# Performance work log

Hardware: AMD Instinct MI355X
Metric: run time of the kernel (lower is better)

Reference implementation:

```python
import jax, jax.numpy as jnp
import numpy as np

# Dims: N batch, C=in=out channels, T frames, V joints, S subsets, R rel_channels, H SE hidden
N, C, T, V = 256, 64, 64, 25
S, R = 3, C // 8           # num_subset, rel_channels = in_channels // rel_reduction
O = C                       # out_channels
H = max(4, O // 4)          # SE attention_channels
BN_EPS = 1e-5


def setup_inputs() -> dict:
    key = jax.random.key(0)
    ks = jax.random.split(key, 12)
    sc = 0.1
    return {
        "x":     jax.random.normal(ks[0], (N, C, T, V), jnp.float32),
        "PA":    jax.random.normal(ks[1], (S, V, V), jnp.float32) * sc,
        "alpha": jnp.ones((S,), jnp.float32),
        # per-subset stacked 1x1-conv weights (kernel_size=1 -> plain matrices)
        "w1": jax.random.normal(ks[2], (S, R, C), jnp.float32) * (2.0 / C) ** 0.5,
        "b1": jnp.zeros((S, R), jnp.float32),
        "w2": jax.random.normal(ks[3], (S, R, C), jnp.float32) * (2.0 / C) ** 0.5,
        "b2": jnp.zeros((S, R), jnp.float32),
        "w3": jax.random.normal(ks[4], (S, O, C), jnp.float32) * (2.0 / C) ** 0.5,
        "b3": jnp.zeros((S, O), jnp.float32),
        "w4": jax.random.normal(ks[5], (S, O, R), jnp.float32) * (2.0 / R) ** 0.5,
        "b4": jnp.zeros((S, O), jnp.float32),
        # final BN (eval mode: running_mean=0, running_var=1)
        "bn_w": jnp.ones((O,), jnp.float32),
        "bn_b": jnp.zeros((O,), jnp.float32),
        # SE channel attention
        "se_w1": jax.random.normal(ks[6], (H, O), jnp.float32) * (2.0 / O) ** 0.5,
        "se_b1": jnp.zeros((H,), jnp.float32),
        "se_w2": jax.random.normal(ks[7], (O, H), jnp.float32) * (2.0 / H) ** 0.5,
        "se_b2": jnp.zeros((O,), jnp.float32),
    }


def reference(x, PA, alpha, w1, b1, w2, b2, w3, b3, w4, b4,
              bn_w, bn_b, se_w1, se_b1, se_w2, se_b2):
    # --- CTRGC for all S subsets at once ---
    # conv1(x).mean(-2) == conv1 applied to x.mean over T (1x1 conv is linear)
    xm = x.mean(axis=2)                                            # [N,C,V]
    x1 = jnp.einsum('ncv,src->nsrv', xm, w1) + b1[None, :, :, None]
    x2 = jnp.einsum('ncv,src->nsrv', xm, w2) + b2[None, :, :, None]
    x3 = jnp.einsum('nctv,soc->nsotv', x, w3) + b3[None, :, :, None, None]
    # outer-difference + tanh attention map: [N,S,R,V(u),V(v)]
    att = jnp.tanh(x1[..., :, None] - x2[..., None, :])
    m = jnp.einsum('nsruv,sor->nsouv', att, w4) + b4[None, :, :, None, None]
    Asym = PA + jnp.swapaxes(PA, -1, -2)                           # A + A^T, [S,V,V]
    m = m * alpha[None, :, None, None, None] + Asym[None, :, None, :, :]
    m = jax.nn.softmax(m, axis=-2)                                 # softmax over u (dim=-2)
    # einsum 'ncuv,nctv->nctu' per subset, summed over subsets
    y = jnp.einsum('nsouv,nsotv->notu', m, x3)                     # [N,O,T,V]
    # --- BatchNorm2d (eval: mean 0, var 1) ---
    y = y / jnp.sqrt(1.0 + BN_EPS) * bn_w[None, :, None, None] + bn_b[None, :, None, None]
    # --- SE channel attention ---
    pooled = y.mean(axis=(2, 3))                                   # [N,O]
    h = jax.nn.relu(pooled @ se_w1.T + se_b1)
    se = jax.nn.sigmoid(h @ se_w2.T + se_b2)
    y = y * se[:, :, None, None]
    # --- residual (in==out -> identity down) + ReLU ---
    return jax.nn.relu(y + x)
```

## Files before the change

### kernel.cpp

```cpp
#include <hip/hip_runtime.h>

#define NN 256
#define CC 64
#define TT 64
#define VV 25
#define SS 3
#define RR 8
#define OO 64
#define HH 16

typedef _Float16 f16;
typedef _Float16 f16x8 __attribute__((ext_vector_type(8)));
typedef float f32x4 __attribute__((ext_vector_type(4)));

#define IBN 0.9999950000374997f

#define MG_NSTRIDE 153600

__device__ __forceinline__ float tanh_fast(float xx) {
  float e = __expf(2.0f * xx);
  return 1.0f - __fdividef(2.0f, e + 1.0f);
}

__device__ __forceinline__ int mti(int mo, int u, int v) {
  return (mo*800 + u*32 + v) ^ ((mo & 6) << 2);
}

__global__ __launch_bounds__(512) void k1(
    const float* __restrict__ x, const float* __restrict__ PA,
    const float* __restrict__ alpha,
    const float* __restrict__ w1, const float* __restrict__ b1,
    const float* __restrict__ w2, const float* __restrict__ b2,
    const float* __restrict__ w3, const float* __restrict__ b3,
    const float* __restrict__ w4, const float* __restrict__ b4,
    const float* __restrict__ bn_w, const float* __restrict__ bn_b,
    const float* __restrict__ se_w1, const float* __restrict__ se_b1,
    const float* __restrict__ se_w2, const float* __restrict__ se_b2,
    f16* __restrict__ m_g, float* __restrict__ se_g, f16* __restrict__ w3p_g)
{
  __shared__ float part[64][8][25];
  __shared__ float xms[1600];
  __shared__ float x1s[600], x2s[600];
  __shared__ float w1s[1536], w2s[1536];
  __shared__ float asym_s[1875];
  __shared__ __attribute__((aligned(16))) float att2[5000];
  __shared__ __attribute__((aligned(16))) f16 mtf[25600];
  __shared__ float xmv[64], pooledv[64], hbuf[16];

  int n = blockIdx.x, tid = threadIdx.x;

  for (int i = tid; i < 1536; i += 512) { w1s[i] = w1[i]; w2s[i] = w2[i]; }
  for (int i = tid; i < 1875; i += 512) {
    int s = i / 625, rem = i - s*625, u = rem / 25, v = rem - u*25;
    asym_s[i] = PA[s*625 + u*25 + v] + PA[s*625 + v*25 + u];
  }
  for (int i = tid; i < 5600; i += 512) {
    int mo = i / 175, rem = i - mo*175, u = rem / 7, v = 25 + (rem - u*7);
    mtf[mti(mo, u, v)] = (f16)0.f;
  }

  {
    int c = tid >> 3, tq = tid & 7;
    const float* p = x + (size_t)(n*64 + c)*1600 + tq*200;
    float acc[25];
    #pragma unroll
    for (int i = 0; i < 25; ++i) acc[i] = 0.f;
    for (int blk = 0; blk < 2; ++blk) {
      const float* pb = p + blk*100;
      #pragma unroll
      for (int j = 0; j < 25; ++j) {
        f32x4 vv = *(const f32x4*)(pb + 4*j);
        acc[(4*j + 0) % 25] += vv[0];
        acc[(4*j + 1) % 25] += vv[1];
        acc[(4*j + 2) % 25] += vv[2];
        acc[(4*j + 3) % 25] += vv[3];
      }
    }
    #pragma unroll
    for (int i = 0; i < 25; ++i) part[c][tq][i] = acc[i];
  }
  __syncthreads();

  for (int idx = tid; idx < 1600; idx += 512) {
    int cc = idx / 25, v = idx - cc*25;
    float s = 0.f;
    #pragma unroll
    for (int tq = 0; tq < 8; ++tq) s += part[cc][tq][v];
    xms[idx] = s * (1.0f/64.0f);
  }
  __syncthreads();

  for (int idx = tid; idx < 600; idx += 512) {
    int sr = idx / 25, v = idx - sr*25;
    float a1 = b1[sr], a2 = b2[sr];
    #pragma unroll
    for (int c = 0; c < 64; ++c) {
      float xv = xms[c*25 + v];
      a1 += xv * w1s[sr*64 + c];
      a2 += xv * w2s[sr*64 + c];
    }
    x1s[idx] = a1; x2s[idx] = a2;
  }

  if (tid < 64) {
    float s = 0.f;
    #pragma unroll
    for (int v = 0; v < 25; ++v) s += xms[tid*25 + v];
    xmv[tid] = s * (1.0f/25.0f);
  }
  __syncthreads();
  if (tid < 64) {
    int o = tid;
    float pp = b3[o] + b3[64 + o] + b3[128 + o];
    for (int cc = 0; cc < 64; ++cc)
      pp += xmv[cc] * (w3[o*64 + cc] + w3[4096 + o*64 + cc] + w3[8192 + o*64 + cc]);
    pooledv[o] = IBN * bn_w[o] * pp + bn_b[o];
  }
  __syncthreads();
  if (tid < 16) {
    float hh = se_b1[tid];
    for (int o = 0; o < 64; ++o) hh += pooledv[o] * se_w1[tid*64 + o];
    hbuf[tid] = fmaxf(hh, 0.0f);
  }
  __syncthreads();
  if (tid < 64) {
    float t = se_b2[tid];
    for (int j = 0; j < 16; ++j) t += hbuf[j] * se_w2[tid*16 + j];
    se_g[n*64 + tid] = 1.0f / (1.0f + __expf(-t));
  }

  f16x8* mg8 = (f16x8*)(m_g + (size_t)n*MG_NSTRIDE);
  for (int s = 0; s < 3; ++s) {
    __syncthreads();
    for (int idx = tid; idx < 5000; idx += 512) {
      int uv = idx >> 3, r = idx & 7;
      int u = uv / 25, v = uv - u*25;
      att2[idx] = tanh_fast(x1s[(s*8 + r)*25 + u] - x2s[(s*8 + r)*25 + v]);
    }
    __syncthreads();

    float alphav = alpha[s];
    for (int oh = 0; oh < 2; ++oh) {
      if (tid < 400) {
        int ot = tid / 25, v = tid - ot*25;
        int o0 = oh*32 + ot*2;
        float w4r[2][8], b4r[2];
        #pragma unroll
        for (int oo = 0; oo < 2; ++oo) {
          b4r[oo] = b4[s*64 + o0 + oo];
          #pragma unroll
          for (int r = 0; r < 8; ++r) w4r[oo][r] = w4[(s*64 + o0 + oo)*8 + r];
        }
        float acc[2][25];
        #pragma unroll
        for (int u = 0; u < 25; ++u) {
          const float* ap = &att2[(u*25 + v)*8];
          f32x4 a0 = *(const f32x4*)ap;
          f32x4 a1 = *(const f32x4*)(ap + 4);
          float asv = asym_s[s*625 + u*25 + v];
          #pragma unroll
          for (int oo = 0; oo < 2; ++oo) {
            float t = b4r[oo];
            t += a0[0]*w4r[oo][0] + a0[1]*w4r[oo][1] + a0[2]*w4r[oo][2] + a0[3]*w4r[oo][3];
            t += a1[0]*w4r[oo][4] + a1[1]*w4r[oo][5] + a1[2]*w4r[oo][6] + a1[3]*w4r[oo][7];
            acc[oo][u] = t*alphav + asv;
          }
        }
        #pragma unroll
        for (int oo = 0; oo < 2; ++oo) {
          int mo = ot*2 + oo;
          float mx = -1e30f;
          #pragma unroll
          for (int u = 0; u < 25; ++u) mx = fmaxf(mx, acc[oo][u]);
          float sum = 0.f;
          #pragma unroll
          for (int u = 0; u < 25; ++u) {
            float e = __expf(acc[oo][u] - mx); acc[oo][u] = e; sum += e;
          }
          float inv = 1.0f / sum;
          #pragma unroll
          for (int u = 0; u < 25; ++u) mtf[mti(mo, u, v)] = (f16)(acc[oo][u]*inv);
        }
      }
      __syncthreads();
      for (int idx = tid; idx < 3200; idx += 512) {
        int mo = idx / 100, rem = idx - mo*100, u = rem >> 2, vc = rem & 3;
        int o = oh*32 + mo;
        f16x8 val = *(const f16x8*)&mtf[mti(mo, u, vc*8)];
        mg8[((size_t)(s*64 + o)*25 + u)*4 + vc] = val;
      }
      __syncthreads();
    }
  }

  if (n == 0) {
    for (int idx = tid; idx < 12288; idx += 512) {
      int j = idx & 7, lane = (idx >> 3) & 63, kk = (idx >> 9) & 1, mi = idx >> 10;
      int s = mi >> 2, o = ((mi & 3) << 4) + (lane & 15);
      int cc = kk*32 + ((lane >> 4) << 3) + j;
      w3p_g[idx] = (f16)w3[(s*64 + o)*64 + cc];
    }
  }
}

struct __align__(16) SmemC {
  f16   xsT[400][72];
  f16   zs[16][16][40];
  float b3s[192];
};

__global__ __launch_bounds__(512, 4) void kc(
    const float* __restrict__ x, const float* __restrict__ b3,
    const float* __restrict__ bn_w, const float* __restrict__ bn_b,
    const f16* __restrict__ m_g, const float* __restrict__ se_g,
    const f16* __restrict__ w3p_g, float* __restrict__ out)
{
  __shared__ SmemC sm;
  int bid = blockIdx.x;
  int xcd = bid & 7, ii = bid >> 3;
  int n = xcd*32 + (ii >> 1), th = ii & 1;
  int tid = threadIdx.x;
  int lane = tid & 63, w = tid >> 6, q = lane >> 4, l15 = lane & 15;

  if (tid < 192) sm.b3s[tid] = b3[tid];
  for (int i = tid; i < 3840; i += 512) {
    int op = i / 240, rem = i - op*240, t = rem / 15, v = 25 + (rem - t*15);
    sm.zs[op][t][v] = (f16)0.f;
  }

  const f16x8* w3pv = (const f16x8*)w3p_g;
  const f16x8* mgv  = (const f16x8*)(m_g + (size_t)n*MG_NSTRIDE);

  for (int tloc = 0; tloc < 2; ++tloc) {
    int tt = th*2 + tloc;
    __syncthreads();

    {
      const float* xb = x + (size_t)n*CC*1600 + tt*400;
      for (int idx = tid; idx < 3200; idx += 512) {
        int cb = idx / 400, j = idx - cb*400;
        f16x8 hv;
        #pragma unroll
        for (int k = 0; k < 8; ++k) hv[k] = (f16)xb[(cb*8 + k)*1600 + j];
        *(f16x8*)&sm.xsT[j][cb*8] = hv;
      }
    }
    __syncthreads();

    for (int ob = 0; ob < 4; ++ob) {
      f32x4 yacc[2][2];
      #pragma unroll
      for (int i = 0; i < 2; ++i) {
        yacc[i][0] = (f32x4){0.f,0.f,0.f,0.f};
        yacc[i][1] = (f32x4){0.f,0.f,0.f,0.f};
      }

      for (int s = 0; s < 3; ++s) {
        f16x8 bm[2][2];
        int u2 = 16 + l15; if (u2 > 24) u2 = 24;
        #pragma unroll
        for (int i = 0; i < 2; ++i) {
          int o = ob*16 + w*2 + i;
          int rb = (s*64 + o)*25;
          bm[i][0] = mgv[(rb + l15)*4 + q];
          bm[i][1] = mgv[(rb + u2)*4 + q];
        }
        int mi = s*4 + ob;
        f16x8 a0 = w3pv[(mi*2 + 0)*64 + lane];
        f16x8 a1 = w3pv[(mi*2 + 1)*64 + lane];

        __syncthreads();

        for (int ni = w; ni < 25; ni += 8) {
          int row = ni*16 + l15;
          f16x8 bf0 = *(const f16x8*)&sm.xsT[row][q*8];
          f16x8 bf1 = *(const f16x8*)&sm.xsT[row][32 + q*8];
          f32x4 acc = (f32x4){0.f,0.f,0.f,0.f};
          acc = __builtin_amdgcn_mfma_f32_16x16x32_f16(a0, bf0, acc, 0, 0, 0);
          acc = __builtin_amdgcn_mfma_f32_16x16x32_f16(a1, bf1, acc, 0, 0, 0);
          int t = row / 25, v = row - t*25;
          #pragma unroll
          for (int rg = 0; rg < 4; ++rg) {
            int op = q*4 + rg;
            sm.zs[op][t][v] = (f16)(acc[rg] + sm.b3s[s*64 + ob*16 + op]);
          }
        }
        __syncthreads();

        #pragma unroll
        for (int i = 0; i < 2; ++i) {
          int op = w*2 + i;
          f16x8 az = *(const f16x8*)&sm.zs[op][l15][q*8];
          yacc[i][0] = __builtin_amdgcn_mfma_f32_16x16x32_f16(az, bm[i][0], yacc[i][0], 0, 0, 0);
          yacc[i][1] = __builtin_amdgcn_mfma_f32_16x16x32_f16(az, bm[i][1], yacc[i][1], 0, 0, 0);
        }
      }

      #pragma unroll
      for (int i = 0; i < 2; ++i) {
        int op = w*2 + i, o = ob*16 + op;
        float sev   = se_g[n*64 + o];
        float scale = IBN * bn_w[o] * sev;
        float bias  = bn_b[o] * sev;
        #pragma unroll
        for (int ut = 0; ut < 2; ++ut) {
          int u = ut*16 + l15;
          if (u < 25) {
            #pragma unroll
            for (int rg = 0; rg < 4; ++rg) {
              int t = q*4 + rg;
              float xres = (float)sm.xsT[t*25 + u][o];
              float val = yacc[i][ut][rg]*scale + bias + xres;
              out[(((size_t)n*64 + o)*64 + tt*16 + t)*25 + u] = fmaxf(val, 0.0f);
            }
          }
        }
      }
    }
  }
}

extern "C" void kernel_launch(void* const* d_in, const int* in_sizes, int n_in,
                              void* d_out, int out_size, void* d_ws, size_t ws_size,
                              hipStream_t stream)
{
  const float* x    = (const float*)d_in[0];
  const float* PA   = (const float*)d_in[1];
  const float* alp  = (const float*)d_in[2];
  const float* w1   = (const float*)d_in[3];
  const float* b1   = (const float*)d_in[4];
  const float* w2   = (const float*)d_in[5];
  const float* b2   = (const float*)d_in[6];
  const float* w3   = (const float*)d_in[7];
  const float* b3   = (const float*)d_in[8];
  const float* w4   = (const float*)d_in[9];
  const float* b4   = (const float*)d_in[10];
  const float* bnw  = (const float*)d_in[11];
  const float* bnb  = (const float*)d_in[12];
  const float* sw1  = (const float*)d_in[13];
  const float* sb1  = (const float*)d_in[14];
  const float* sw2  = (const float*)d_in[15];
  const float* sb2  = (const float*)d_in[16];

  char* ws = (char*)d_ws;
  f16*   m_g   = (f16*)ws;
  float* se_g  = (float*)(ws + 78643200);
  f16*   w3p_g = (f16*)(ws + 78643200 + 65536);

  float* out = (float*)d_out;

  k1<<<256, 512, 0, stream>>>(x, PA, alp, w1, b1, w2, b2, w3, b3, w4, b4,
                              bnw, bnb, sw1, sb1, sw2, sb2, m_g, se_g, w3p_g);
  kc<<<512, 512, 0, stream>>>(x, b3, bnw, bnb, m_g, se_g, w3p_g, out);
}
```

Baseline: 327.6 us.

## Fuse attention-map computation into the graph-conv kernel, dropping global m buffer

```diff
diff --git a/kernel.cpp b/kernel.cpp
--- a/kernel.cpp
+++ b/kernel.cpp
@@ -15,18 +15,28 @@
 
 #define IBN 0.9999950000374997f
 
-#define MG_NSTRIDE 153600
-
 __device__ __forceinline__ float tanh_fast(float xx) {
   float e = __expf(2.0f * xx);
   return 1.0f - __fdividef(2.0f, e + 1.0f);
 }
 
-__device__ __forceinline__ int mti(int mo, int u, int v) {
-  return (mo*800 + u*32 + v) ^ ((mo & 6) << 2);
-}
-
-__global__ __launch_bounds__(512) void k1(
+struct __align__(16) SmemF {
+  union { f16 xsT[400][72]; float part[64][8][25]; } u1;
+  f16 zs[16][16][40];
+  f16 mt[16][25][40];
+  union { f16 att2h[15000]; float w12[3072]; } u2;
+  float asym[1875];
+  float xms[1600];
+  float x1s[600];
+  float x2s[600];
+  float b3s[192];
+  float sev[64];
+  float pooledv[64];
+  float hbuf[16];
+  float xmv[64];
+};
+
+__global__ __launch_bounds__(512) void kf(
     const float* __restrict__ x, const float* __restrict__ PA,
     const float* __restrict__ alpha,
     const float* __restrict__ w1, const float* __restrict__ b1,
@@ -36,27 +46,27 @@
     const float* __restrict__ bn_w, const float* __restrict__ bn_b,
     const float* __restrict__ se_w1, const float* __restrict__ se_b1,
     const float* __restrict__ se_w2, const float* __restrict__ se_b2,
-    f16* __restrict__ m_g, float* __restrict__ se_g, f16* __restrict__ w3p_g)
+    float* __restrict__ out)
 {
-  __shared__ float part[64][8][25];
-  __shared__ float xms[1600];
-  __shared__ float x1s[600], x2s[600];
-  __shared__ float w1s[1536], w2s[1536];
-  __shared__ float asym_s[1875];
-  __shared__ __attribute__((aligned(16))) float att2[5000];
-  __shared__ __attribute__((aligned(16))) f16 mtf[25600];
-  __shared__ float xmv[64], pooledv[64], hbuf[16];
-
+  __shared__ SmemF sm;
   int n = blockIdx.x, tid = threadIdx.x;
-
-  for (int i = tid; i < 1536; i += 512) { w1s[i] = w1[i]; w2s[i] = w2[i]; }
+  int lane = tid & 63, w = tid >> 6, q = lane >> 4, l15 = lane & 15;
+
+  for (int i = tid; i < 1536; i += 512) {
+    sm.u2.w12[i] = w1[i]; sm.u2.w12[1536 + i] = w2[i];
+  }
   for (int i = tid; i < 1875; i += 512) {
     int s = i / 625, rem = i - s*625, u = rem / 25, v = rem - u*25;
-    asym_s[i] = PA[s*625 + u*25 + v] + PA[s*625 + v*25 + u];
-  }
-  for (int i = tid; i < 5600; i += 512) {
-    int mo = i / 175, rem = i - mo*175, u = rem / 7, v = 25 + (rem - u*7);
-    mtf[mti(mo, u, v)] = (f16)0.f;
+    sm.asym[i] = PA[s*625 + u*25 + v] + PA[s*625 + v*25 + u];
+  }
+  if (tid < 192) sm.b3s[tid] = b3[tid];
+  for (int i = tid; i < 3840; i += 512) {
+    int op = i / 240, rem = i - op*240, t = rem / 15, v = 25 + (rem - t*15);
+    sm.zs[op][t][v] = (f16)0.f;
+  }
+  for (int i = tid; i < 2800; i += 512) {
+    int o = i / 175, rem = i - o*175, u = rem / 7, v = 25 + (rem - u*7);
+    sm.mt[o][u][v] = (f16)0.f;
   }
 
   {
@@ -77,7 +87,7 @@
       }
     }
     #pragma unroll
-    for (int i = 0; i < 25; ++i) part[c][tq][i] = acc[i];
+    for (int i = 0; i < 25; ++i) sm.u1.part[c][tq][i] = acc[i];
   }
   __syncthreads();
 
@@ -85,8 +95,8 @@
     int cc = idx / 25, v = idx - cc*25;
     float s = 0.f;
     #pragma unroll
-    for (int tq = 0; tq < 8; ++tq) s += part[cc][tq][v];
-    xms[idx] = s * (1.0f/64.0f);
+    for (int tq = 0; tq < 8; ++tq) s += sm.u1.part[cc][tq][v];
+    sm.xms[idx] = s * (1.0f/64.0f);
   }
   __syncthreads();
 
@@ -95,154 +105,59 @@
     float a1 = b1[sr], a2 = b2[sr];
     #pragma unroll
     for (int c = 0; c < 64; ++c) {
-      float xv = xms[c*25 + v];
-      a1 += xv * w1s[sr*64 + c];
-      a2 += xv * w2s[sr*64 + c];
-    }
-    x1s[idx] = a1; x2s[idx] = a2;
-  }
-
+      float xv = sm.xms[c*25 + v];
+      a1 += xv * sm.u2.w12[sr*64 + c];
+      a2 += xv * sm.u2.w12[1536 + sr*64 + c];
+    }
+    sm.x1s[idx] = a1; sm.x2s[idx] = a2;
+  }
   if (tid < 64) {
     float s = 0.f;
     #pragma unroll
-    for (int v = 0; v < 25; ++v) s += xms[tid*25 + v];
-    xmv[tid] = s * (1.0f/25.0f);
-  }
-  __syncthreads();
+    for (int v = 0; v < 25; ++v) s += sm.xms[tid*25 + v];
+    sm.xmv[tid] = s * (1.0f/25.0f);
+  }
+  __syncthreads();
+
+  for (int idx = tid; idx < 15000; idx += 512) {
+    int sA = idx / 5000, rem = idx - sA*5000;
+    int uv = rem >> 3, r = rem & 7;
+    int u = uv / 25, v = uv - u*25;
+    sm.u2.att2h[idx] =
+        (f16)tanh_fast(sm.x1s[(sA*8 + r)*25 + u] - sm.x2s[(sA*8 + r)*25 + v]);
+  }
   if (tid < 64) {
     int o = tid;
     float pp = b3[o] + b3[64 + o] + b3[128 + o];
     for (int cc = 0; cc < 64; ++cc)
-      pp += xmv[cc] * (w3[o*64 + cc] + w3[4096 + o*64 + cc] + w3[8192 + o*64 + cc]);
-    pooledv[o] = IBN * bn_w[o] * pp + bn_b[o];
+      pp += sm.xmv[cc] * (w3[o*64 + cc] + w3[4096 + o*64 + cc] + w3[8192 + o*64 + cc]);
+    sm.pooledv[o] = IBN * bn_w[o] * pp + bn_b[o];
   }
   __syncthreads();
   if (tid < 16) {
     float hh = se_b1[tid];
-    for (int o = 0; o < 64; ++o) hh += pooledv[o] * se_w1[tid*64 + o];
-    hbuf[tid] = fmaxf(hh, 0.0f);
+    for (int o = 0; o < 64; ++o) hh += sm.pooledv[o] * se_w1[tid*64 + o];
+    sm.hbuf[tid] = fmaxf(hh, 0.0f);
   }
   __syncthreads();
   if (tid < 64) {
     float t = se_b2[tid];
-    for (int j = 0; j < 16; ++j) t += hbuf[j] * se_w2[tid*16 + j];
-    se_g[n*64 + tid] = 1.0f / (1.0f + __expf(-t));
-  }
-
-  f16x8* mg8 = (f16x8*)(m_g + (size_t)n*MG_NSTRIDE);
-  for (int s = 0; s < 3; ++s) {
+    for (int j = 0; j < 16; ++j) t += sm.hbuf[j] * se_w2[tid*16 + j];
+    sm.sev[tid] = 1.0f / (1.0f + __expf(-t));
+  }
+
+  const size_t xbase = (size_t)n*64*1600;
+  for (int tloc = 0; tloc < 4; ++tloc) {
     __syncthreads();
-    for (int idx = tid; idx < 5000; idx += 512) {
-      int uv = idx >> 3, r = idx & 7;
-      int u = uv / 25, v = uv - u*25;
-      att2[idx] = tanh_fast(x1s[(s*8 + r)*25 + u] - x2s[(s*8 + r)*25 + v]);
-    }
-    __syncthreads();
-
-    float alphav = alpha[s];
-    for (int oh = 0; oh < 2; ++oh) {
-      if (tid < 400) {
-        int ot = tid / 25, v = tid - ot*25;
-        int o0 = oh*32 + ot*2;
-        float w4r[2][8], b4r[2];
-        #pragma unroll
-        for (int oo = 0; oo < 2; ++oo) {
-          b4r[oo] = b4[s*64 + o0 + oo];
-          #pragma unroll
-          for (int r = 0; r < 8; ++r) w4r[oo][r] = w4[(s*64 + o0 + oo)*8 + r];
-        }
-        float acc[2][25];
-        #pragma unroll
-        for (int u = 0; u < 25; ++u) {
-          const float* ap = &att2[(u*25 + v)*8];
-          f32x4 a0 = *(const f32x4*)ap;
-          f32x4 a1 = *(const f32x4*)(ap + 4);
-          float asv = asym_s[s*625 + u*25 + v];
-          #pragma unroll
-          for (int oo = 0; oo < 2; ++oo) {
-            float t = b4r[oo];
-            t += a0[0]*w4r[oo][0] + a0[1]*w4r[oo][1] + a0[2]*w4r[oo][2] + a0[3]*w4r[oo][3];
-            t += a1[0]*w4r[oo][4] + a1[1]*w4r[oo][5] + a1[2]*w4r[oo][6] + a1[3]*w4r[oo][7];
-            acc[oo][u] = t*alphav + asv;
-          }
-        }
-        #pragma unroll
-        for (int oo = 0; oo < 2; ++oo) {
-          int mo = ot*2 + oo;
-          float mx = -1e30f;
-          #pragma unroll
-          for (int u = 0; u < 25; ++u) mx = fmaxf(mx, acc[oo][u]);
-          float sum = 0.f;
-          #pragma unroll
-          for (int u = 0; u < 25; ++u) {
-            float e = __expf(acc[oo][u] - mx); acc[oo][u] = e; sum += e;
-          }
-          float inv = 1.0f / sum;
-          #pragma unroll
-          for (int u = 0; u < 25; ++u) mtf[mti(mo, u, v)] = (f16)(acc[oo][u]*inv);
-        }
-      }
-      __syncthreads();
-      for (int idx = tid; idx < 3200; idx += 512) {
-        int mo = idx / 100, rem = idx - mo*100, u = rem >> 2, vc = rem & 3;
-        int o = oh*32 + mo;
-        f16x8 val = *(const f16x8*)&mtf[mti(mo, u, vc*8)];
-        mg8[((size_t)(s*64 + o)*25 + u)*4 + vc] = val;
-      }
-      __syncthreads();
-    }
-  }
-
-  if (n == 0) {
-    for (int idx = tid; idx < 12288; idx += 512) {
-      int j = idx & 7, lane = (idx >> 3) & 63, kk = (idx >> 9) & 1, mi = idx >> 10;
-      int s = mi >> 2, o = ((mi & 3) << 4) + (lane & 15);
-      int cc = kk*32 + ((lane >> 4) << 3) + j;
-      w3p_g[idx] = (f16)w3[(s*64 + o)*64 + cc];
-    }
-  }
-}
-
-struct __align__(16) SmemC {
-  f16   xsT[400][72];
-  f16   zs[16][16][40];
-  float b3s[192];
-};
-
-__global__ __launch_bounds__(512, 4) void kc(
-    const float* __restrict__ x, const float* __restrict__ b3,
-    const float* __restrict__ bn_w, const float* __restrict__ bn_b,
-    const f16* __restrict__ m_g, const float* __restrict__ se_g,
-    const f16* __restrict__ w3p_g, float* __restrict__ out)
-{
-  __shared__ SmemC sm;
-  int bid = blockIdx.x;
-  int xcd = bid & 7, ii = bid >> 3;
-  int n = xcd*32 + (ii >> 1), th = ii & 1;
-  int tid = threadIdx.x;
-  int lane = tid & 63, w = tid >> 6, q = lane >> 4, l15 = lane & 15;
-
-  if (tid < 192) sm.b3s[tid] = b3[tid];
-  for (int i = tid; i < 3840; i += 512) {
-    int op = i / 240, rem = i - op*240, t = rem / 15, v = 25 + (rem - t*15);
-    sm.zs[op][t][v] = (f16)0.f;
-  }
-
-  const f16x8* w3pv = (const f16x8*)w3p_g;
-  const f16x8* mgv  = (const f16x8*)(m_g + (size_t)n*MG_NSTRIDE);
-
-  for (int tloc = 0; tloc < 2; ++tloc) {
-    int tt = th*2 + tloc;
-    __syncthreads();
 
     {
-      const float* xb = x + (size_t)n*CC*1600 + tt*400;
+      const float* xb = x + xbase + tloc*400;
       for (int idx = tid; idx < 3200; idx += 512) {
         int cb = idx / 400, j = idx - cb*400;
         f16x8 hv;
         #pragma unroll
         for (int k = 0; k < 8; ++k) hv[k] = (f16)xb[(cb*8 + k)*1600 + j];
-        *(f16x8*)&sm.xsT[j][cb*8] = hv;
+        *(f16x8*)&sm.u1.xsT[j][cb*8] = hv;
       }
     }
     __syncthreads();
@@ -256,25 +171,54 @@
       }
 
       for (int s = 0; s < 3; ++s) {
-        f16x8 bm[2][2];
-        int u2 = 16 + l15; if (u2 > 24) u2 = 24;
-        #pragma unroll
-        for (int i = 0; i < 2; ++i) {
-          int o = ob*16 + w*2 + i;
-          int rb = (s*64 + o)*25;
-          bm[i][0] = mgv[(rb + l15)*4 + q];
-          bm[i][1] = mgv[(rb + u2)*4 + q];
-        }
-        int mi = s*4 + ob;
-        f16x8 a0 = w3pv[(mi*2 + 0)*64 + lane];
-        f16x8 a1 = w3pv[(mi*2 + 1)*64 + lane];
-
         __syncthreads();
+
+        const float* wr = w3 + ((s*64 + ob*16 + l15) << 6) + q*8;
+        f32x4 wa = *(const f32x4*)(wr);
+        f32x4 wb = *(const f32x4*)(wr + 4);
+        f32x4 wc = *(const f32x4*)(wr + 32);
+        f32x4 wd = *(const f32x4*)(wr + 36);
+        f16x8 a0, a1;
+        #pragma unroll
+        for (int k = 0; k < 4; ++k) {
+          a0[k] = (f16)wa[k]; a0[4 + k] = (f16)wb[k];
+          a1[k] = (f16)wc[k]; a1[4 + k] = (f16)wd[k];
+        }
+
+        if (tid < 400) {
+          int ot = tid / 25, v = tid - ot*25;
+          int og = s*64 + ob*16 + ot;
+          float alphav = alpha[s];
+          float b4r = b4[og];
+          float w4r[8];
+          #pragma unroll
+          for (int r = 0; r < 8; ++r) w4r[r] = w4[og*8 + r];
+          float acc[25];
+          #pragma unroll
+          for (int u = 0; u < 25; ++u) {
+            f16x8 av = *(const f16x8*)&sm.u2.att2h[s*5000 + (u*25 + v)*8];
+            float t = b4r;
+            #pragma unroll
+            for (int r = 0; r < 8; ++r) t += (float)av[r] * w4r[r];
+            acc[u] = t*alphav + sm.asym[s*625 + u*25 + v];
+          }
+          float mx = -1e30f;
+          #pragma unroll
+          for (int u = 0; u < 25; ++u) mx = fmaxf(mx, acc[u]);
+          float sum = 0.f;
+          #pragma unroll
+          for (int u = 0; u < 25; ++u) {
+            float e = __expf(acc[u] - mx); acc[u] = e; sum += e;
+          }
+          float inv = 1.0f / sum;
+          #pragma unroll
+          for (int u = 0; u < 25; ++u) sm.mt[ot][u][v] = (f16)(acc[u]*inv);
+        }
 
         for (int ni = w; ni < 25; ni += 8) {
           int row = ni*16 + l15;
-          f16x8 bf0 = *(const f16x8*)&sm.xsT[row][q*8];
-          f16x8 bf1 = *(const f16x8*)&sm.xsT[row][32 + q*8];
+          f16x8 bf0 = *(const f16x8*)&sm.u1.xsT[row][q*8];
+          f16x8 bf1 = *(const f16x8*)&sm.u1.xsT[row][32 + q*8];
           f32x4 acc = (f32x4){0.f,0.f,0.f,0.f};
           acc = __builtin_amdgcn_mfma_f32_16x16x32_f16(a0, bf0, acc, 0, 0, 0);
           acc = __builtin_amdgcn_mfma_f32_16x16x32_f16(a1, bf1, acc, 0, 0, 0);
@@ -287,21 +231,24 @@
         }
         __syncthreads();
 
+        int uc = 16 + l15; if (uc > 24) uc = 24;
         #pragma unroll
         for (int i = 0; i < 2; ++i) {
           int op = w*2 + i;
-          f16x8 az = *(const f16x8*)&sm.zs[op][l15][q*8];
-          yacc[i][0] = __builtin_amdgcn_mfma_f32_16x16x32_f16(az, bm[i][0], yacc[i][0], 0, 0, 0);
-          yacc[i][1] = __builtin_amdgcn_mfma_f32_16x16x32_f16(az, bm[i][1], yacc[i][1], 0, 0, 0);
+          f16x8 az  = *(const f16x8*)&sm.zs[op][l15][q*8];
+          f16x8 bm0 = *(const f16x8*)&sm.mt[op][l15][q*8];
+          f16x8 bm1 = *(const f16x8*)&sm.mt[op][uc][q*8];
+          yacc[i][0] = __builtin_amdgcn_mfma_f32_16x16x32_f16(az, bm0, yacc[i][0], 0, 0, 0);
+          yacc[i][1] = __builtin_amdgcn_mfma_f32_16x16x32_f16(az, bm1, yacc[i][1], 0, 0, 0);
         }
       }
 
       #pragma unroll
       for (int i = 0; i < 2; ++i) {
         int op = w*2 + i, o = ob*16 + op;
-        float sev   = se_g[n*64 + o];
-        float scale = IBN * bn_w[o] * sev;
-        float bias  = bn_b[o] * sev;
+        float se    = sm.sev[o];
+        float scale = IBN * bn_w[o] * se;
+        float bias  = bn_b[o] * se;
         #pragma unroll
         for (int ut = 0; ut < 2; ++ut) {
           int u = ut*16 + l15;
@@ -309,9 +256,9 @@
             #pragma unroll
             for (int rg = 0; rg < 4; ++rg) {
               int t = q*4 + rg;
-              float xres = (float)sm.xsT[t*25 + u][o];
+              float xres = (float)sm.u1.xsT[t*25 + u][o];
               float val = yacc[i][ut][rg]*scale + bias + xres;
-              out[(((size_t)n*64 + o)*64 + tt*16 + t)*25 + u] = fmaxf(val, 0.0f);
+              out[(((size_t)n*64 + o)*64 + tloc*16 + t)*25 + u] = fmaxf(val, 0.0f);
             }
           }
         }
@@ -342,14 +289,8 @@
   const float* sw2  = (const float*)d_in[15];
   const float* sb2  = (const float*)d_in[16];
 
-  char* ws = (char*)d_ws;
-  f16*   m_g   = (f16*)ws;
-  float* se_g  = (float*)(ws + 78643200);
-  f16*   w3p_g = (f16*)(ws + 78643200 + 65536);
-
   float* out = (float*)d_out;
 
-  k1<<<256, 512, 0, stream>>>(x, PA, alp, w1, b1, w2, b2, w3, b3, w4, b4,
-                              bnw, bnb, sw1, sb1, sw2, sb2, m_g, se_g, w3p_g);
-  kc<<<512, 512, 0, stream>>>(x, b3, bnw, bnb, m_g, se_g, w3p_g, out);
+  kf<<<256, 512, 0, stream>>>(x, PA, alp, w1, b1, w2, b2, w3, b3, w4, b4,
+                              bnw, bnb, sw1, sb1, sw2, sb2, out);
 }
```

Result: slower. 416.1 us (+27.0%).
